# Performance work log

Hardware: AMD Instinct MI355X
Metric: run time of the kernel (lower is better)

The kernel has to match this reference:

```python
import jax, jax.numpy as jnp
import numpy as np

B, T, C, H = 2, 2048, 1024, 16
D = C // H  # head_dim = 64

def setup_inputs() -> dict:
    key = jax.random.key(0)
    k1, k2, k3, k4, k5 = jax.random.split(key, 5)
    x = jax.random.normal(k1, (B, T, C), dtype=jnp.float32)
    # RoPE tables (realistic frequencies)
    inv_freq = 1.0 / (10000.0 ** (jnp.arange(0, D // 2, dtype=jnp.float32) / (D // 2)))
    pos = jnp.arange(T, dtype=jnp.float32)
    ang = pos[:, None] * inv_freq[None, :]          # (T, D/2)
    cos, sin = jnp.cos(ang), jnp.sin(ang)
    # causal mask (True = keep)
    mask = jnp.tril(jnp.ones((T, T), dtype=bool))
    W_qkv = jax.random.normal(k2, (3 * C, C), dtype=jnp.float32) * (1.0 / np.sqrt(C))
    W_out = jax.random.normal(k3, (C, C), dtype=jnp.float32) * (1.0 / np.sqrt(C))
    return {"x": x, "cos": cos, "sin": sin, "mask": mask, "W_qkv": W_qkv, "W_out": W_out}

def apply_rope(x, cos, sin):
    # x: (B, H, T, D); cos/sin: (T, D/2)
    d = x.shape[-1] // 2
    x1, x2 = x[..., :d], x[..., d:]
    c = cos[None, None, :x.shape[2], :]
    s = sin[None, None, :x.shape[2], :]
    return jnp.concatenate([x1 * c - x2 * s, x2 * c + x1 * s], axis=-1)

def reference(x, cos, sin, mask, W_qkv, W_out):
    b, t, c = x.shape
    qkv = (x @ W_qkv.T).reshape(b, t, 3, H, D)
    q, k, v = qkv[:, :, 0], qkv[:, :, 1], qkv[:, :, 2]   # (b, t, H, D)
    q = q.transpose(0, 2, 1, 3)
    k = k.transpose(0, 2, 1, 3)
    v = v.transpose(0, 2, 1, 3)                           # (b, H, t, D)
    q = apply_rope(q, cos, sin)
    k = apply_rope(k, cos, sin)
    attn = jnp.einsum('bhqd,bhkd->bhqk', q, k) / jnp.sqrt(jnp.asarray(D, x.dtype))
    attn = jnp.where(mask[None, None, :, :], attn, -jnp.inf)
    attn = jax.nn.softmax(attn, axis=-1)
    out = jnp.einsum('bhqk,bhkd->bhqd', attn, v)          # (b, H, t, D)
    out = out.transpose(0, 2, 1, 3).reshape(b, t, c)
    return out @ W_out.T
```

## Files before the change

### kernel.cpp

```cpp
#include <hip/hip_runtime.h>
#include <stdint.h>

typedef __bf16 bf16;
typedef __bf16 bf16x4 __attribute__((ext_vector_type(4)));
typedef __bf16 bf16x8 __attribute__((ext_vector_type(8)));
typedef float f32x4 __attribute__((ext_vector_type(4)));

#define TSEQ 2048
#define NHEAD 16
#define HDIM 64
#define CDIM 1024

#define AS1(p) ((const __attribute__((address_space(1))) void*)(p))
#define AS3(p) ((__attribute__((address_space(3))) void*)(p))

#if __has_builtin(__builtin_amdgcn_exp2f)
#define EXP2(x) __builtin_amdgcn_exp2f(x)
#else
#define EXP2(x) exp2f(x)
#endif

__global__ __launch_bounds__(256) void cast3_bf16(const float* __restrict__ in1, int n1,
                                                  const float* __restrict__ in2, int n2,
                                                  const float* __restrict__ in3, int n3,
                                                  bf16* __restrict__ out1,
                                                  bf16* __restrict__ out2,
                                                  bf16* __restrict__ out3) {
  int i = (blockIdx.x * 256 + threadIdx.x) * 8;
  const float* src;
  bf16* dst;
  if (i < n1) {
    src = in1 + i; dst = out1 + i;
  } else if (i < n1 + n2) {
    src = in2 + (i - n1); dst = out2 + (i - n1);
  } else if (i < n1 + n2 + n3) {
    src = in3 + (i - n1 - n2); dst = out3 + (i - n1 - n2);
  } else {
    return;
  }
  float4 a = *(const float4*)src;
  float4 b = *(const float4*)(src + 4);
  bf16x8 r;
  r[0] = (bf16)a.x; r[1] = (bf16)a.y; r[2] = (bf16)a.z; r[3] = (bf16)a.w;
  r[4] = (bf16)b.x; r[5] = (bf16)b.y; r[6] = (bf16)b.z; r[7] = (bf16)b.w;
  *(bf16x8*)dst = r;
}

__global__ __launch_bounds__(256) void gemm_qkv_rope(const bf16* __restrict__ A,
                                                     const bf16* __restrict__ B,
                                                     const float* __restrict__ cosb,
                                                     const float* __restrict__ sinb,
                                                     bf16* __restrict__ Qb,
                                                     bf16* __restrict__ Kb,
                                                     bf16* __restrict__ Vt) {
  constexpr int K = 1024;
  __shared__ bf16 smem[8704];
  const int t = threadIdx.x;
  const int w = t >> 6, l = t & 63, g = l >> 4, ln = l & 15;
  const int wm = (w >> 1) * 64, wn = (w & 1) * 64;
  const int m0 = blockIdx.x * 128, n0 = blockIdx.y * 128;
  const int r0 = t >> 2, kc0 = (t & 3) * 8;

  f32x4 acc[4][4] = {};

  for (int k0 = 0; k0 < K; k0 += 32) {
    __syncthreads();
    __builtin_amdgcn_global_load_lds(AS1(A + (size_t)(m0 + r0) * K + k0 + kc0),
                                     AS3(&smem[t * 8]), 16, 0, 0);
    __builtin_amdgcn_global_load_lds(AS1(A + (size_t)(m0 + r0 + 64) * K + k0 + kc0),
                                     AS3(&smem[(t + 256) * 8]), 16, 0, 0);
    __builtin_amdgcn_global_load_lds(AS1(B + (size_t)(n0 + r0) * K + k0 + kc0),
                                     AS3(&smem[4096 + t * 8]), 16, 0, 0);
    __builtin_amdgcn_global_load_lds(AS1(B + (size_t)(n0 + r0 + 64) * K + k0 + kc0),
                                     AS3(&smem[4096 + (t + 256) * 8]), 16, 0, 0);
    __syncthreads();
    bf16x8 af[4], bfr[4];
#pragma unroll
    for (int i = 0; i < 4; i++) {
      af[i] = *(const bf16x8*)&smem[(wm + i * 16 + ln) * 32 + g * 8];
      bfr[i] = *(const bf16x8*)&smem[4096 + (wn + i * 16 + ln) * 32 + g * 8];
    }
#pragma unroll
    for (int i = 0; i < 4; i++)
#pragma unroll
      for (int j = 0; j < 4; j++)
        acc[i][j] = __builtin_amdgcn_mfma_f32_16x16x32_bf16(af[i], bfr[j], acc[i][j], 0, 0, 0);
  }

  const int part = n0 >> 10;
  if (part < 2) {
    bf16* dst = part ? Kb : Qb;
    const float qs = part ? 1.0f : 0.18033688011112042f;
#pragma unroll
    for (int i = 0; i < 4; i++)
#pragma unroll
      for (int j = 0; j < 2; j++) {
        int nl = (n0 & 1023) + wn + j * 16 + ln;
        int h = nl >> 6, d = nl & 31;
#pragma unroll
        for (int r = 0; r < 4; r++) {
          int row = m0 + wm + i * 16 + g * 4 + r;
          int tok = row & (TSEQ - 1), bb = row >> 11;
          float c = cosb[tok * 32 + d], s = sinb[tok * 32 + d];
          float a1 = acc[i][j][r], a2 = acc[i][j + 2][r];
          size_t ob = ((size_t)(bb * NHEAD + h) * TSEQ + tok) * HDIM + d;
          dst[ob] = (bf16)((a1 * c - a2 * s) * qs);
          dst[ob + 32] = (bf16)((a2 * c + a1 * s) * qs);
        }
      }
  } else {
    const int bb = m0 >> 11;
    const int tbase = m0 & (TSEQ - 1);
    const int nbase = n0 - 2048;
#pragma unroll
    for (int pass = 0; pass < 2; pass++) {
      __syncthreads();
      if ((w >> 1) == pass) {
#pragma unroll
        for (int i = 0; i < 4; i++)
#pragma unroll
          for (int j = 0; j < 4; j++) {
            int lr = i * 16 + g * 4;
            int lc = wn + j * 16 + ln;
#pragma unroll
            for (int r = 0; r < 4; r++)
              smem[(lr + r) * 132 + lc] = (bf16)acc[i][j][r];
          }
      }
      __syncthreads();
      for (int c = t; c < 1024; c += 256) {
        int ch = c >> 3, tc = c & 7;
        bf16x8 o;
#pragma unroll
        for (int j2 = 0; j2 < 8; j2++) o[j2] = smem[(tc * 8 + j2) * 132 + ch];
        int n = nbase + ch;
        int h = n >> 6, d = n & 63;
        *(bf16x8*)(Vt + ((size_t)((bb * NHEAD + h) * HDIM + d)) * TSEQ +
                   tbase + pass * 64 + tc * 8) = o;
      }
    }
  }
}

__global__ __launch_bounds__(256) void gemm_out(const bf16* __restrict__ A,
                                                const bf16* __restrict__ B,
                                                float* __restrict__ C,
                                                int M, int N, int K) {
  __shared__ bf16 As[64 * 32];
  __shared__ bf16 Bs[128 * 32];
  const int t = threadIdx.x;
  const int w = t >> 6, l = t & 63, g = l >> 4, ln = l & 15;
  const int m0 = blockIdx.x * 64, n0 = blockIdx.y * 128;
  const int r0 = t >> 2, kc0 = (t & 3) * 8;

  f32x4 acc[4][2] = {};

  for (int k0 = 0; k0 < K; k0 += 32) {
    __syncthreads();
    __builtin_amdgcn_global_load_lds(AS1(A + (size_t)(m0 + r0) * K + k0 + kc0),
                                     AS3(&As[t * 8]), 16, 0, 0);
    __builtin_amdgcn_global_load_lds(AS1(B + (size_t)(n0 + r0) * K + k0 + kc0),
                                     AS3(&Bs[t * 8]), 16, 0, 0);
    __builtin_amdgcn_global_load_lds(AS1(B + (size_t)(n0 + r0 + 64) * K + k0 + kc0),
                                     AS3(&Bs[(t + 256) * 8]), 16, 0, 0);
    __syncthreads();
    bf16x8 af[4], bfr[2];
#pragma unroll
    for (int i = 0; i < 4; i++)
      af[i] = *(const bf16x8*)&As[(i * 16 + ln) * 32 + g * 8];
#pragma unroll
    for (int j = 0; j < 2; j++)
      bfr[j] = *(const bf16x8*)&Bs[(w * 32 + j * 16 + ln) * 32 + g * 8];
#pragma unroll
    for (int i = 0; i < 4; i++)
#pragma unroll
      for (int j = 0; j < 2; j++)
        acc[i][j] = __builtin_amdgcn_mfma_f32_16x16x32_bf16(af[i], bfr[j], acc[i][j], 0, 0, 0);
  }
#pragma unroll
  for (int i = 0; i < 4; i++)
#pragma unroll
    for (int j = 0; j < 2; j++) {
      int row = m0 + i * 16 + g * 4;
      int col = n0 + w * 32 + j * 16 + ln;
#pragma unroll
      for (int r = 0; r < 4; r++)
        C[(size_t)(row + r) * N + col] = acc[i][j][r];
    }
}

__global__ __launch_bounds__(512) void attn_fwd(const bf16* __restrict__ Q,
                                                const bf16* __restrict__ K,
                                                const bf16* __restrict__ Vt,
                                                bf16* __restrict__ ctx) {
  __shared__ bf16 Ks[2][64 * 72];
  __shared__ bf16 VTs[2][64 * 72];
  __shared__ bf16 Ps[8][16 * 72];
  __shared__ float Mrg[4][64][16];
  __shared__ float lred[4][16];
  __shared__ float linv[4][16];

  const int t = threadIdx.x;
  const int gp = t >> 8;
  const int tl = t & 255;
  const int w = t >> 6;
  const int w2 = w & 3;
  const int l = t & 63, g = l >> 4, ln = l & 15;
  const int bid = blockIdx.x;
  const int bh = bid & 31, pr = bid >> 5;
  const size_t base = (size_t)bh * TSEQ * HDIM;

  const int r0 = tl >> 3, r1 = (tl + 256) >> 3, ch0 = (tl & 7) * 8;
  bf16x8 kr0, kr1, vr0, vr1;

  for (int half = 0; half < 2; half++) {
    const int qb = half ? (31 - pr) : pr;
    const int q0 = qb * 64;
    const int q_global = q0 + w2 * 16 + ln;
    bf16x8 bq[2];
    bq[0] = *(const bf16x8*)(Q + base + (size_t)q_global * HDIM + g * 8);
    bq[1] = *(const bf16x8*)(Q + base + (size_t)q_global * HDIM + 32 + g * 8);
    f32x4 acc[4] = {};
    float l_run = 0.f;
    const int nit = (qb >> 1) + 1;

    if (gp <= qb) {
      kr0 = *(const bf16x8*)(K + base + (size_t)(gp * 64 + r0) * HDIM + ch0);
      kr1 = *(const bf16x8*)(K + base + (size_t)(gp * 64 + r1) * HDIM + ch0);
      vr0 = *(const bf16x8*)(Vt + base + (size_t)r0 * TSEQ + gp * 64 + ch0);
      vr1 = *(const bf16x8*)(Vt + base + (size_t)r1 * TSEQ + gp * 64 + ch0);
    }

    for (int i = 0; i < nit; i++) {
      const int kt = 2 * i + gp;
      const bool active = (kt <= qb);
      __syncthreads();
      if (active) {
        *(bf16x8*)&Ks[gp][r0 * 72 + ch0] = kr0;
        *(bf16x8*)&Ks[gp][r1 * 72 + ch0] = kr1;
        *(bf16x8*)&VTs[gp][r0 * 72 + ch0] = vr0;
        *(bf16x8*)&VTs[gp][r1 * 72 + ch0] = vr1;
      }
      __syncthreads();
      const int ktn = kt + 2;
      if (ktn <= qb) {
        kr0 = *(const bf16x8*)(K + base + (size_t)(ktn * 64 + r0) * HDIM + ch0);
        kr1 = *(const bf16x8*)(K + base + (size_t)(ktn * 64 + r1) * HDIM + ch0);
        vr0 = *(const bf16x8*)(Vt + base + (size_t)r0 * TSEQ + ktn * 64 + ch0);
        vr1 = *(const bf16x8*)(Vt + base + (size_t)r1 * TSEQ + ktn * 64 + ch0);
      }
      if (active) {
        f32x4 st[4] = {};
#pragma unroll
        for (int step = 0; step < 2; step++)
#pragma unroll
          for (int mt = 0; mt < 4; mt++) {
            bf16x8 ak = *(const bf16x8*)&Ks[gp][(mt * 16 + ln) * 72 + step * 32 + g * 8];
            st[mt] = __builtin_amdgcn_mfma_f32_16x16x32_bf16(ak, bq[step], st[mt], 0, 0, 0);
          }
        float vals[16];
        if (kt == qb) {
#pragma unroll
          for (int mt = 0; mt < 4; mt++)
#pragma unroll
            for (int r = 0; r < 4; r++) {
              int kg = kt * 64 + mt * 16 + g * 4 + r;
              vals[mt * 4 + r] = (kg <= q_global) ? fminf(st[mt][r], 60.f) : -INFINITY;
            }
        } else {
#pragma unroll
          for (int mt = 0; mt < 4; mt++)
#pragma unroll
            for (int r = 0; r < 4; r++) vals[mt * 4 + r] = fminf(st[mt][r], 60.f);
        }
        float psum = 0.f;
#pragma unroll
        for (int i2 = 0; i2 < 16; i2++) {
          float p = EXP2(vals[i2]);
          vals[i2] = p;
          psum += p;
        }
        psum += __shfl_xor(psum, 16);
        psum += __shfl_xor(psum, 32);
        l_run += psum;
#pragma unroll
        for (int mt = 0; mt < 4; mt++) {
          bf16x4 pk;
#pragma unroll
          for (int r = 0; r < 4; r++) pk[r] = (bf16)vals[mt * 4 + r];
          *(bf16x4*)&Ps[w][ln * 72 + mt * 16 + g * 4] = pk;
        }
#pragma unroll
        for (int step = 0; step < 2; step++) {
          bf16x8 ap = *(const bf16x8*)&Ps[w][ln * 72 + step * 32 + g * 8];
#pragma unroll
          for (int nt = 0; nt < 4; nt++) {
            bf16x8 bv = *(const bf16x8*)&VTs[gp][(nt * 16 + ln) * 72 + step * 32 + g * 8];
            acc[nt] = __builtin_amdgcn_mfma_f32_16x16x32_bf16(ap, bv, acc[nt], 0, 0, 0);
          }
        }
      }
    }
    __syncthreads();
    if (gp == 1) {
#pragma unroll
      for (int nt = 0; nt < 4; nt++) *(f32x4*)&Mrg[w2][l][nt * 4] = acc[nt];
      if (l < 16) lred[w2][ln] = l_run;
    }
    __syncthreads();
    if (gp == 0) {
#pragma unroll
      for (int nt = 0; nt < 4; nt++) acc[nt] += *(const f32x4*)&Mrg[w2][l][nt * 4];
      float ltot = l_run + lred[w2][ln];
      if (l < 16) linv[w2][ln] = 1.0f / ltot;
      float lrow[4];
#pragma unroll
      for (int r = 0; r < 4; r++) lrow[r] = linv[w2][g * 4 + r];
      const int b = bh >> 4, h = bh & (NHEAD - 1);
#pragma unroll
      for (int nt = 0; nt < 4; nt++)
#pragma unroll
        for (int r = 0; r < 4; r++) {
          int q = q0 + w2 * 16 + g * 4 + r;
          ctx[(size_t)(b * TSEQ + q) * CDIM + h * HDIM + nt * 16 + ln] =
              (bf16)(acc[nt][r] * lrow[r]);
        }
    }
  }
}

extern "C" void kernel_launch(void* const* d_in, const int* in_sizes, int n_in,
                              void* d_out, int out_size, void* d_ws, size_t ws_size,
                              hipStream_t stream) {
  const float* x = (const float*)d_in[0];
  const float* cosb = (const float*)d_in[1];
  const float* sinb = (const float*)d_in[2];
  const float* Wqkv = (const float*)d_in[4];
  const float* Wout = (const float*)d_in[5];
  float* out = (float*)d_out;

  char* ws = (char*)d_ws;
  bf16* x_bf = (bf16*)ws;
  bf16* ctx = (bf16*)ws;
  bf16* Wqkv_bf = (bf16*)(ws + 8388608);
  bf16* Wout_bf = (bf16*)(ws + 14680064);
  bf16* Qb = (bf16*)(ws + 16777216);
  bf16* Kb = (bf16*)(ws + 25165824);
  bf16* Vt = (bf16*)(ws + 33554432);

  cast3_bf16<<<(4194304 + 3145728 + 1048576) / 8 / 256, 256, 0, stream>>>(
      x, 4194304, Wqkv, 3145728, Wout, 1048576, x_bf, Wqkv_bf, Wout_bf);
  gemm_qkv_rope<<<dim3(32, 24), 256, 0, stream>>>(x_bf, Wqkv_bf, cosb, sinb, Qb, Kb, Vt);
  attn_fwd<<<512, 512, 0, stream>>>(Qb, Kb, Vt, ctx);
  gemm_out<<<dim3(64, 8), 256, 0, stream>>>(ctx, Wout_bf, out, 4096, 1024, 1024);
}
```

Measured before the change: 187.8 us.

## Split attention into one block per query tile, dropping paired tiles and KV split

```diff
diff --git a/kernel.cpp b/kernel.cpp
--- a/kernel.cpp
+++ b/kernel.cpp
@@ -189,144 +189,122 @@
     }
 }
 
-__global__ __launch_bounds__(512) void attn_fwd(const bf16* __restrict__ Q,
+__global__ __launch_bounds__(256) void attn_fwd(const bf16* __restrict__ Q,
                                                 const bf16* __restrict__ K,
                                                 const bf16* __restrict__ Vt,
                                                 bf16* __restrict__ ctx) {
-  __shared__ bf16 Ks[2][64 * 72];
-  __shared__ bf16 VTs[2][64 * 72];
-  __shared__ bf16 Ps[8][16 * 72];
-  __shared__ float Mrg[4][64][16];
-  __shared__ float lred[4][16];
-  __shared__ float linv[4][16];
+  __shared__ bf16 Ks[64 * 72];
+  __shared__ bf16 VTs[64 * 72];
+  __shared__ bf16 Ps[4][16 * 72];
 
   const int t = threadIdx.x;
-  const int gp = t >> 8;
-  const int tl = t & 255;
   const int w = t >> 6;
-  const int w2 = w & 3;
   const int l = t & 63, g = l >> 4, ln = l & 15;
   const int bid = blockIdx.x;
-  const int bh = bid & 31, pr = bid >> 5;
+  const int bh = bid & 31;
+  const int qb = 31 - (bid >> 5);
   const size_t base = (size_t)bh * TSEQ * HDIM;
 
-  const int r0 = tl >> 3, r1 = (tl + 256) >> 3, ch0 = (tl & 7) * 8;
-  bf16x8 kr0, kr1, vr0, vr1;
-
-  for (int half = 0; half < 2; half++) {
-    const int qb = half ? (31 - pr) : pr;
-    const int q0 = qb * 64;
-    const int q_global = q0 + w2 * 16 + ln;
-    bf16x8 bq[2];
-    bq[0] = *(const bf16x8*)(Q + base + (size_t)q_global * HDIM + g * 8);
-    bq[1] = *(const bf16x8*)(Q + base + (size_t)q_global * HDIM + 32 + g * 8);
-    f32x4 acc[4] = {};
-    float l_run = 0.f;
-    const int nit = (qb >> 1) + 1;
-
-    if (gp <= qb) {
-      kr0 = *(const bf16x8*)(K + base + (size_t)(gp * 64 + r0) * HDIM + ch0);
-      kr1 = *(const bf16x8*)(K + base + (size_t)(gp * 64 + r1) * HDIM + ch0);
-      vr0 = *(const bf16x8*)(Vt + base + (size_t)r0 * TSEQ + gp * 64 + ch0);
-      vr1 = *(const bf16x8*)(Vt + base + (size_t)r1 * TSEQ + gp * 64 + ch0);
-    }
-
-    for (int i = 0; i < nit; i++) {
-      const int kt = 2 * i + gp;
-      const bool active = (kt <= qb);
-      __syncthreads();
-      if (active) {
-        *(bf16x8*)&Ks[gp][r0 * 72 + ch0] = kr0;
-        *(bf16x8*)&Ks[gp][r1 * 72 + ch0] = kr1;
-        *(bf16x8*)&VTs[gp][r0 * 72 + ch0] = vr0;
-        *(bf16x8*)&VTs[gp][r1 * 72 + ch0] = vr1;
-      }
-      __syncthreads();
-      const int ktn = kt + 2;
-      if (ktn <= qb) {
-        kr0 = *(const bf16x8*)(K + base + (size_t)(ktn * 64 + r0) * HDIM + ch0);
-        kr1 = *(const bf16x8*)(K + base + (size_t)(ktn * 64 + r1) * HDIM + ch0);
-        vr0 = *(const bf16x8*)(Vt + base + (size_t)r0 * TSEQ + ktn * 64 + ch0);
-        vr1 = *(const bf16x8*)(Vt + base + (size_t)r1 * TSEQ + ktn * 64 + ch0);
-      }
-      if (active) {
-        f32x4 st[4] = {};
-#pragma unroll
-        for (int step = 0; step < 2; step++)
-#pragma unroll
-          for (int mt = 0; mt < 4; mt++) {
-            bf16x8 ak = *(const bf16x8*)&Ks[gp][(mt * 16 + ln) * 72 + step * 32 + g * 8];
-            st[mt] = __builtin_amdgcn_mfma_f32_16x16x32_bf16(ak, bq[step], st[mt], 0, 0, 0);
-          }
-        float vals[16];
-        if (kt == qb) {
-#pragma unroll
-          for (int mt = 0; mt < 4; mt++)
-#pragma unroll
-            for (int r = 0; r < 4; r++) {
-              int kg = kt * 64 + mt * 16 + g * 4 + r;
-              vals[mt * 4 + r] = (kg <= q_global) ? fminf(st[mt][r], 60.f) : -INFINITY;
-            }
-        } else {
-#pragma unroll
-          for (int mt = 0; mt < 4; mt++)
-#pragma unroll
-            for (int r = 0; r < 4; r++) vals[mt * 4 + r] = fminf(st[mt][r], 60.f);
+  const int r0 = t >> 3, ch0 = (t & 7) * 8;
+  const int q0 = qb * 64;
+  const int q_global = q0 + w * 16 + ln;
+  const int px = (ln & 8) ? 32 : 0;
+
+  bf16x8 bq[2];
+  bq[0] = *(const bf16x8*)(Q + base + (size_t)q_global * HDIM + g * 8);
+  bq[1] = *(const bf16x8*)(Q + base + (size_t)q_global * HDIM + 32 + g * 8);
+
+  const bf16* kp0 = K + base + (size_t)r0 * HDIM + ch0;
+  const bf16* kp1 = K + base + (size_t)(r0 + 32) * HDIM + ch0;
+  const bf16* vp0 = Vt + base + (size_t)r0 * TSEQ + ch0;
+  const bf16* vp1 = Vt + base + (size_t)(r0 + 32) * TSEQ + ch0;
+
+  bf16x8 kr0 = *(const bf16x8*)kp0;
+  bf16x8 kr1 = *(const bf16x8*)kp1;
+  bf16x8 vr0 = *(const bf16x8*)vp0;
+  bf16x8 vr1 = *(const bf16x8*)vp1;
+
+  f32x4 acc[4] = {};
+  float l_run = 0.f;
+
+  for (int kt = 0; kt <= qb; kt++) {
+    __syncthreads();
+    *(bf16x8*)&Ks[r0 * 72 + ch0] = kr0;
+    *(bf16x8*)&Ks[(r0 + 32) * 72 + ch0] = kr1;
+    *(bf16x8*)&VTs[r0 * 72 + ch0] = vr0;
+    *(bf16x8*)&VTs[(r0 + 32) * 72 + ch0] = vr1;
+    __syncthreads();
+    if (kt < qb) {
+      kr0 = *(const bf16x8*)(kp0 + (kt + 1) * 64 * HDIM);
+      kr1 = *(const bf16x8*)(kp1 + (kt + 1) * 64 * HDIM);
+      vr0 = *(const bf16x8*)(vp0 + (kt + 1) * 64);
+      vr1 = *(const bf16x8*)(vp1 + (kt + 1) * 64);
+    }
+
+    f32x4 st[4] = {};
+#pragma unroll
+    for (int step = 0; step < 2; step++)
+#pragma unroll
+      for (int mt = 0; mt < 4; mt++) {
+        bf16x8 ak = *(const bf16x8*)&Ks[(mt * 16 + ln) * 72 + step * 32 + g * 8];
+        st[mt] = __builtin_amdgcn_mfma_f32_16x16x32_bf16(ak, bq[step], st[mt], 0, 0, 0);
+      }
+    float vals[16];
+    if (kt == qb) {
+#pragma unroll
+      for (int mt = 0; mt < 4; mt++)
+#pragma unroll
+        for (int r = 0; r < 4; r++) {
+          int kg = kt * 64 + mt * 16 + g * 4 + r;
+          vals[mt * 4 + r] = (kg <= q_global) ? fminf(st[mt][r], 60.f) : -INFINITY;
         }
-        float psum = 0.f;
-#pragma unroll
-        for (int i2 = 0; i2 < 16; i2++) {
-          float p = EXP2(vals[i2]);
-          vals[i2] = p;
-          psum += p;
-        }
-        psum += __shfl_xor(psum, 16);
-        psum += __shfl_xor(psum, 32);
-        l_run += psum;
-#pragma unroll
-        for (int mt = 0; mt < 4; mt++) {
-          bf16x4 pk;
-#pragma unroll
-          for (int r = 0; r < 4; r++) pk[r] = (bf16)vals[mt * 4 + r];
-          *(bf16x4*)&Ps[w][ln * 72 + mt * 16 + g * 4] = pk;
-        }
-#pragma unroll
-        for (int step = 0; step < 2; step++) {
-          bf16x8 ap = *(const bf16x8*)&Ps[w][ln * 72 + step * 32 + g * 8];
-#pragma unroll
-          for (int nt = 0; nt < 4; nt++) {
-            bf16x8 bv = *(const bf16x8*)&VTs[gp][(nt * 16 + ln) * 72 + step * 32 + g * 8];
-            acc[nt] = __builtin_amdgcn_mfma_f32_16x16x32_bf16(ap, bv, acc[nt], 0, 0, 0);
-          }
-        }
-      }
-    }
-    __syncthreads();
-    if (gp == 1) {
-#pragma unroll
-      for (int nt = 0; nt < 4; nt++) *(f32x4*)&Mrg[w2][l][nt * 4] = acc[nt];
-      if (l < 16) lred[w2][ln] = l_run;
-    }
-    __syncthreads();
-    if (gp == 0) {
-#pragma unroll
-      for (int nt = 0; nt < 4; nt++) acc[nt] += *(const f32x4*)&Mrg[w2][l][nt * 4];
-      float ltot = l_run + lred[w2][ln];
-      if (l < 16) linv[w2][ln] = 1.0f / ltot;
-      float lrow[4];
-#pragma unroll
-      for (int r = 0; r < 4; r++) lrow[r] = linv[w2][g * 4 + r];
-      const int b = bh >> 4, h = bh & (NHEAD - 1);
-#pragma unroll
-      for (int nt = 0; nt < 4; nt++)
-#pragma unroll
-        for (int r = 0; r < 4; r++) {
-          int q = q0 + w2 * 16 + g * 4 + r;
-          ctx[(size_t)(b * TSEQ + q) * CDIM + h * HDIM + nt * 16 + ln] =
-              (bf16)(acc[nt][r] * lrow[r]);
-        }
-    }
-  }
+    } else {
+#pragma unroll
+      for (int mt = 0; mt < 4; mt++)
+#pragma unroll
+        for (int r = 0; r < 4; r++) vals[mt * 4 + r] = fminf(st[mt][r], 60.f);
+    }
+    float psum = 0.f;
+#pragma unroll
+    for (int i2 = 0; i2 < 16; i2++) {
+      float p = EXP2(vals[i2]);
+      vals[i2] = p;
+      psum += p;
+    }
+    psum += __shfl_xor(psum, 16);
+    psum += __shfl_xor(psum, 32);
+    l_run += psum;
+#pragma unroll
+    for (int mt = 0; mt < 4; mt++) {
+      bf16x4 pk;
+#pragma unroll
+      for (int r = 0; r < 4; r++) pk[r] = (bf16)vals[mt * 4 + r];
+      *(bf16x4*)&Ps[w][ln * 72 + ((mt * 16 + g * 4) ^ px)] = pk;
+    }
+#pragma unroll
+    for (int step = 0; step < 2; step++) {
+      bf16x8 ap = *(const bf16x8*)&Ps[w][ln * 72 + ((step * 32 + g * 8) ^ px)];
+#pragma unroll
+      for (int nt = 0; nt < 4; nt++) {
+        bf16x8 bv = *(const bf16x8*)&VTs[(nt * 16 + ln) * 72 + step * 32 + g * 8];
+        acc[nt] = __builtin_amdgcn_mfma_f32_16x16x32_bf16(ap, bv, acc[nt], 0, 0, 0);
+      }
+    }
+  }
+
+  float inv = 1.0f / l_run;
+  float lrow[4];
+#pragma unroll
+  for (int r = 0; r < 4; r++) lrow[r] = __shfl(inv, g * 4 + r, 64);
+  const int b = bh >> 4, h = bh & (NHEAD - 1);
+#pragma unroll
+  for (int nt = 0; nt < 4; nt++)
+#pragma unroll
+    for (int r = 0; r < 4; r++) {
+      int q = q0 + w * 16 + g * 4 + r;
+      ctx[(size_t)(b * TSEQ + q) * CDIM + h * HDIM + nt * 16 + ln] =
+          (bf16)(acc[nt][r] * lrow[r]);
+    }
 }
 
 extern "C" void kernel_launch(void* const* d_in, const int* in_sizes, int n_in,
@@ -351,6 +329,6 @@
   cast3_bf16<<<(4194304 + 3145728 + 1048576) / 8 / 256, 256, 0, stream>>>(
       x, 4194304, Wqkv, 3145728, Wout, 1048576, x_bf, Wqkv_bf, Wout_bf);
   gemm_qkv_rope<<<dim3(32, 24), 256, 0, stream>>>(x_bf, Wqkv_bf, cosb, sinb, Qb, Kb, Vt);
-  attn_fwd<<<512, 512, 0, stream>>>(Qb, Kb, Vt, ctx);
+  attn_fwd<<<1024, 256, 0, stream>>>(Qb, Kb, Vt, ctx);
   gemm_out<<<dim3(64, 8), 256, 0, stream>>>(ctx, Wout_bf, out, 4096, 1024, 1024);
 }
```

After: 191.0 us. Within noise of the previous version (+1.7%).
